# Performance work log

Hardware: AMD Instinct MI355X
Metric: run time of the kernel (lower is better)

## Reference

```python
import jax, jax.numpy as jnp
import numpy as np

DIM = 1024
NUM_HEADS = 16
HEAD_DIM = DIM // NUM_HEADS


def setup_inputs() -> dict:
    key = jax.random.key(0)
    k1, k2, k3 = jax.random.split(key, 3)
    x = jax.random.normal(k1, (2, 2048, DIM), dtype=jnp.float32)
    # nn.Linear weights stored as [out, in]; apply as x @ W.T
    w_qkv = jax.random.normal(k2, (3 * DIM, DIM), dtype=jnp.float32) * (1.0 / np.sqrt(DIM))
    w_out = jax.random.normal(k3, (DIM, DIM), dtype=jnp.float32) * (1.0 / np.sqrt(DIM))
    return {"x": x, "w_qkv": w_qkv, "w_out": w_out}


def reference(x, w_qkv, w_out):
    b, t, _ = x.shape
    qkv = x @ w_qkv.T                                  # [b, t, 3*dim]
    qkv = qkv.reshape(b, t, 3, NUM_HEADS, HEAD_DIM)    # (three h d) split order
    q, k, v = jnp.moveaxis(qkv, 2, 0)                  # each [b, t, h, d]
    q = q.transpose(0, 2, 1, 3)                        # [b, h, t, d]
    k = k.transpose(0, 2, 1, 3)
    v = v.transpose(0, 2, 1, 3)
    attn = jnp.einsum('bhid,bhjd->bhij', q, k) / np.sqrt(HEAD_DIM)
    causal_mask = jnp.triu(jnp.ones((t, t), dtype=bool), k=1)
    attn = jnp.where(causal_mask, -jnp.inf, attn)
    attn = jax.nn.softmax(attn, axis=-1)
    out = jnp.einsum('bhij,bhjd->bhid', attn, v)
    out = out.transpose(0, 2, 1, 3).reshape(b, t, DIM)
    return out @ w_out.T
```

## Files before the change

### kernel.cpp

```cpp
#include <hip/hip_runtime.h>

#define DIM_ 1024
#define HEADS_ 16
#define HD_ 64
#define T_ 2048
#define BATCH_ 2
#define QKVN_ 3072

typedef unsigned short u16;
typedef unsigned int u32;
typedef float f32x4 __attribute__((ext_vector_type(4)));
typedef float f32x16 __attribute__((ext_vector_type(16)));
typedef short s16x8 __attribute__((ext_vector_type(8)));
typedef unsigned short u16x4 __attribute__((ext_vector_type(4)));

__device__ __forceinline__ u16 f2bf(float f) {
  unsigned u = __float_as_uint(f);
  u += 0x7fffu + ((u >> 16) & 1u);
  return (u16)(u >> 16);
}

__device__ __forceinline__ float fexp2(float x) {
  float r;
  asm("v_exp_f32 %0, %1" : "=v"(r) : "v"(x));
  return r;
}

__device__ __forceinline__ u32 cvtpk(float a, float b) {
  u32 r;
  asm("v_cvt_pk_bf16_f32 %0, %1, %2" : "=v"(r) : "v"(a), "v"(b));
  return r;
}

__global__ __launch_bounds__(256) void cvt_all(const float* __restrict__ x,
                                               const float* __restrict__ wqkv,
                                               const float* __restrict__ wout,
                                               u16* __restrict__ outbase) {
  int i = blockIdx.x * 256 + threadIdx.x;
  const float4* src;
  int off;
  if (i < 1048576) { src = (const float4*)x; off = i; }
  else if (i < 1835008) { src = (const float4*)wqkv; off = i - 1048576; }
  else { src = (const float4*)wout; off = i - 1835008; }
  float4 v = src[off];
  u16x4 o;
  o.x = f2bf(v.x); o.y = f2bf(v.y); o.z = f2bf(v.z); o.w = f2bf(v.w);
  reinterpret_cast<u16x4*>(outbase)[i] = o;
}

__device__ __forceinline__ void gld_lds16(const void* g, void* l) {
  auto gp = (__attribute__((address_space(1))) char*)(unsigned long long)g;
  auto lp = (__attribute__((address_space(3))) char*)(unsigned int)(unsigned long long)l;
  __builtin_amdgcn_global_load_lds(gp, lp, 16, 0, 0);
}

template <int MODE>
__global__ __launch_bounds__(256) void gemm2(const u16* __restrict__ A,
                                             const u16* __restrict__ B,
                                             void* __restrict__ Cv,
                                             u16* __restrict__ vto,
                                             int N) {
  __shared__ __align__(16) u16 smem[17408];
  u16* As = smem;
  u16* Bs = smem + 8192;
  const int K = 1024;

  const int bid = blockIdx.x;
  const int cpx = gridDim.x >> 3;
  const int swz = (bid & 7) * cpx + (bid >> 3);
  const int nt = swz >> 5, mt = swz & 31;

  const int tid = threadIdx.x;
  const int lane = tid & 63;
  const int w = tid >> 6;
  const int wr = w >> 1, wc = w & 1;
  const int lrow = lane & 15, kg = lane >> 4;
  const u16* Ag = A + (size_t)(mt * 128) * K;
  const u16* Bg = B + (size_t)(nt * 128) * K;

  f32x4 acc[4][4];
#pragma unroll
  for (int i = 0; i < 4; ++i)
#pragma unroll
    for (int j = 0; j < 4; ++j) {
      f32x4 z = {0.f, 0.f, 0.f, 0.f};
      acc[i][j] = z;
    }

  const int e0 = tid * 8;
  const int row0 = e0 >> 5, kc0 = e0 & 31;
  const int row1 = row0 + 64, kc1 = kc0;
  const int ldsoff0 = (tid & ~63) * 16;
  const int ldsoff1 = (256 + (tid & ~63)) * 16;

  gld_lds16(Ag + (size_t)row0 * K + kc0, (char*)As + ldsoff0);
  gld_lds16(Ag + (size_t)row1 * K + kc1, (char*)As + ldsoff1);
  gld_lds16(Bg + (size_t)row0 * K + kc0, (char*)Bs + ldsoff0);
  gld_lds16(Bg + (size_t)row1 * K + kc1, (char*)Bs + ldsoff1);
  __syncthreads();

  int cur = 0;
  for (int k0 = 0; k0 < K; k0 += 32) {
    if (k0 + 32 < K) {
      const int nb = (cur ^ 1) * 8192;
      gld_lds16(Ag + (size_t)row0 * K + k0 + 32 + kc0, (char*)As + nb + ldsoff0);
      gld_lds16(Ag + (size_t)row1 * K + k0 + 32 + kc1, (char*)As + nb + ldsoff1);
      gld_lds16(Bg + (size_t)row0 * K + k0 + 32 + kc0, (char*)Bs + nb + ldsoff0);
      gld_lds16(Bg + (size_t)row1 * K + k0 + 32 + kc1, (char*)Bs + nb + ldsoff1);
    }
    const int cb = cur * 4096;
    s16x8 a[4], b[4];
#pragma unroll
    for (int mf = 0; mf < 4; ++mf)
      a[mf] = *(const s16x8*)&As[cb + (wr * 64 + mf * 16 + lrow) * 32 + 8 * kg];
#pragma unroll
    for (int nf = 0; nf < 4; ++nf)
      b[nf] = *(const s16x8*)&Bs[cb + (wc * 64 + nf * 16 + lrow) * 32 + 8 * kg];
#pragma unroll
    for (int mf = 0; mf < 4; ++mf)
#pragma unroll
      for (int nf = 0; nf < 4; ++nf)
        acc[mf][nf] = __builtin_amdgcn_mfma_f32_16x16x32_bf16(a[mf], b[nf], acc[mf][nf], 0, 0, 0);
    __syncthreads();
    cur ^= 1;
  }

  if (MODE == 1) {
    float* C = (float*)Cv;
#pragma unroll
    for (int mf = 0; mf < 4; ++mf)
#pragma unroll
      for (int nf = 0; nf < 4; ++nf)
#pragma unroll
        for (int j = 0; j < 4; ++j) {
          int r = mt * 128 + wr * 64 + mf * 16 + 4 * kg + j;
          int c = nt * 128 + wc * 64 + nf * 16 + lrow;
          C[(size_t)r * N + c] = acc[mf][nf][j];
        }
  } else if (nt < 16) {
    u16* qkvo = (u16*)Cv;
#pragma unroll
    for (int mf = 0; mf < 4; ++mf)
#pragma unroll
      for (int nf = 0; nf < 4; ++nf)
#pragma unroll
        for (int j = 0; j < 4; ++j) {
          int r = mt * 128 + wr * 64 + mf * 16 + 4 * kg + j;
          int c = nt * 128 + wc * 64 + nf * 16 + lrow;
          qkvo[(size_t)r * QKVN_ + c] = f2bf(acc[mf][nf][j]);
        }
  } else {
    u16* Vlds = smem;
#pragma unroll
    for (int mf = 0; mf < 4; ++mf)
#pragma unroll
      for (int nf = 0; nf < 4; ++nf) {
        const int cl = wc * 64 + nf * 16 + lrow;
        const int rl = wr * 64 + mf * 16 + 4 * kg;
#pragma unroll
        for (int j = 0; j < 4; ++j)
          Vlds[cl * 136 + rl + j] = f2bf(acc[mf][nf][j]);
      }
    __syncthreads();
    const int c16 = tid >> 4, chunk = tid & 15;
    const int bb = mt >> 4;
    const int tb = (mt & 15) * 128 + chunk * 8;
#pragma unroll
    for (int pass = 0; pass < 8; ++pass) {
      const int cl = pass * 16 + c16;
      const int cg = nt * 128 + cl;
      const int hV = (cg >> 6) & 15, d = cg & 63;
      const s16x8 v = *(const s16x8*)&Vlds[cl * 136 + chunk * 8];
      *(s16x8*)(vto + ((size_t)((bb * 16 + hV) * 64 + d)) * T_ + tb) = v;
    }
  }
}

__global__ __launch_bounds__(256, 2) void attn_fwd(const u16* __restrict__ qkv,
                                                   const u16* __restrict__ vt,
                                                   u16* __restrict__ o) {
  const int gid = blockIdx.x;
  const int pr = gid >> 5;
  const int bh = gid & 31;
  const int b = bh >> 4, h = bh & 15;
  const int tid = threadIdx.x;
  const int lane = tid & 63;
  const int qw = (tid >> 6) & 1;
  const int kvg = tid >> 7;
  const int l31 = lane & 31, hi = lane >> 5;

  __shared__ __align__(16) char smem[65536];

  const int row_s = tid >> 3, slot_s = tid & 7;
  const u16* Kbase = qkv + (size_t)(b * T_) * QKVN_ + 1024 + h * 64;
  const u16* Vbase = vt + (size_t)(bh * 64) * T_;
  const u16* KgA = Kbase + (size_t)row_s * QKVN_ + slot_s * 8;
  const u16* KgB = KgA + (size_t)32 * QKVN_;
  const u16* VgA = Vbase + (size_t)row_s * T_ + slot_s * 8;
  const u16* VgB = VgA + (size_t)32 * T_;
  const int dstA = row_s * 128 + ((slot_s ^ (row_s & 7)) << 4);

  const int rbyte = l31 * 128;
  const int xsw = l31 & 7;
  const float CEXP = 0.18033688011112042f;

  for (int ph = 0; ph < 2; ++ph) {
    const int jt = (ph == 0) ? (31 - pr) : pr;
    const int nt = jt + 1;
    const int nrt = (nt + 1) >> 1;
    const int qrow0 = 64 * jt + 32 * qw;

    s16x8 qf[4];
    {
      const u16* qp = qkv + (size_t)(b * T_ + qrow0 + l31) * QKVN_ + h * 64 + 8 * hi;
#pragma unroll
      for (int ksl = 0; ksl < 4; ++ksl)
        qf[ksl] = *(const s16x8*)(qp + 16 * ksl);
    }

    f32x16 o0v, o1v;
#pragma unroll
    for (int r = 0; r < 16; ++r) { o0v[r] = 0.f; o1v[r] = 0.f; }
    float mrun = -__builtin_inff(), lrun = 0.0f;

    __syncthreads();
    *(s16x8*)(smem + dstA)                 = *(const s16x8*)KgA;
    *(s16x8*)(smem + 4096 + dstA)          = *(const s16x8*)KgB;
    *(s16x8*)(smem + 32768 + dstA)         = *(const s16x8*)VgA;
    *(s16x8*)(smem + 32768 + 4096 + dstA)  = *(const s16x8*)VgB;
    if (nt > 1) {
      *(s16x8*)(smem + 8192 + dstA)                = *(const s16x8*)(KgA + (size_t)64 * QKVN_);
      *(s16x8*)(smem + 8192 + 4096 + dstA)         = *(const s16x8*)(KgB + (size_t)64 * QKVN_);
      *(s16x8*)(smem + 32768 + 8192 + dstA)        = *(const s16x8*)(VgA + 64);
      *(s16x8*)(smem + 32768 + 8192 + 4096 + dstA) = *(const s16x8*)(VgB + 64);
    }

    int cur = 0;
    for (int r = 0; r < nrt; ++r) {
      const int t = 2 * r + kvg;
      const bool pe = (2 * r + 2 < nt), po = (2 * r + 3 < nt);
      s16x8 ke0, ke1, ve0, ve1, ko0, ko1, vo0, vo1;
      if (pe) {
        const size_t kofs = (size_t)(2 * r + 2) * 64 * QKVN_;
        const int vofs = (2 * r + 2) * 64;
        ke0 = *(const s16x8*)(KgA + kofs);
        ke1 = *(const s16x8*)(KgB + kofs);
        ve0 = *(const s16x8*)(VgA + vofs);
        ve1 = *(const s16x8*)(VgB + vofs);
      }
      if (po) {
        const size_t kofs = (size_t)(2 * r + 3) * 64 * QKVN_;
        const int vofs = (2 * r + 3) * 64;
        ko0 = *(const s16x8*)(KgA + kofs);
        ko1 = *(const s16x8*)(KgB + kofs);
        vo0 = *(const s16x8*)(VgA + vofs);
        vo1 = *(const s16x8*)(VgB + vofs);
      }
      __syncthreads();

      if (t < nt) {
        const char* Kc = smem + cur * 16384 + kvg * 8192;
        const char* Vc = smem + 32768 + cur * 16384 + kvg * 8192;
        const bool isdiag = (t == nt - 1);
        const bool two = !(isdiag && qw == 0);

        f32x16 s0v, s1v;
#pragma unroll
        for (int rr = 0; rr < 16; ++rr) { s0v[rr] = 0.f; s1v[rr] = 0.f; }
        __builtin_amdgcn_s_setprio(1);
#pragma unroll
        for (int ksl = 0; ksl < 4; ++ksl) {
          const s16x8 kf = *(const s16x8*)(Kc + rbyte + (((2 * ksl + hi) ^ xsw) << 4));
          s0v = __builtin_amdgcn_mfma_f32_32x32x16_bf16(kf, qf[ksl], s0v, 0, 0, 0);
        }
        if (two) {
#pragma unroll
          for (int ksl = 0; ksl < 4; ++ksl) {
            const s16x8 kf = *(const s16x8*)(Kc + 4096 + rbyte + (((2 * ksl + hi) ^ xsw) << 4));
            s1v = __builtin_amdgcn_mfma_f32_32x32x16_bf16(kf, qf[ksl], s1v, 0, 0, 0);
          }
        }
        __builtin_amdgcn_s_setprio(0);

        if (isdiag) {
          const int thr = 32 * qw + l31;
#pragma unroll
          for (int rr = 0; rr < 16; ++rr) {
            const int kvl = 4 * hi + (rr & 3) + 8 * (rr >> 2);
            if (kvl > thr) s0v[rr] = -__builtin_inff();
            if (two && kvl + 32 > thr) s1v[rr] = -__builtin_inff();
          }
        }

        float mloc = s0v[0];
#pragma unroll
        for (int rr = 1; rr < 16; ++rr) mloc = fmaxf(mloc, s0v[rr]);
        if (two) {
#pragma unroll
          for (int rr = 0; rr < 16; ++rr) mloc = fmaxf(mloc, s1v[rr]);
        }
        mloc = fmaxf(mloc, __shfl_xor(mloc, 32));

        const bool needfull = !((mloc - mrun) * CEXP <= 8.0f);
        if (__any(needfull)) {
          const float newm = fmaxf(mrun, mloc);
          const float sc = fexp2((mrun - newm) * CEXP);
          mrun = newm;
          lrun *= sc;
          o0v *= sc;
          o1v *= sc;
        }
        const float msc = mrun * CEXP;

        float rs = 0.0f;
        u32 pd0[8], pd1[8];
#pragma unroll
        for (int ri = 0; ri < 8; ++ri) {
          const float p0 = fexp2(__builtin_fmaf(s0v[2 * ri], CEXP, -msc));
          const float p1 = fexp2(__builtin_fmaf(s0v[2 * ri + 1], CEXP, -msc));
          rs += p0 + p1;
          pd0[ri] = cvtpk(p0, p1);
        }
        if (two) {
#pragma unroll
          for (int ri = 0; ri < 8; ++ri) {
            const float p0 = fexp2(__builtin_fmaf(s1v[2 * ri], CEXP, -msc));
            const float p1 = fexp2(__builtin_fmaf(s1v[2 * ri + 1], CEXP, -msc));
            rs += p0 + p1;
            pd1[ri] = cvtpk(p0, p1);
          }
        }
        rs += __shfl_xor(rs, 32);
        lrun += rs;

        __builtin_amdgcn_s_setprio(1);
#pragma unroll
        for (int kk = 0; kk < 4; ++kk) {
          if (kk >= 2 && !two) break;
          u32 x0, y0, x1, y1;
          if (kk == 0)      { x0 = pd0[0]; y0 = pd0[2]; x1 = pd0[1]; y1 = pd0[3]; }
          else if (kk == 1) { x0 = pd0[4]; y0 = pd0[6]; x1 = pd0[5]; y1 = pd0[7]; }
          else if (kk == 2) { x0 = pd1[0]; y0 = pd1[2]; x1 = pd1[1]; y1 = pd1[3]; }
          else              { x0 = pd1[4]; y0 = pd1[6]; x1 = pd1[5]; y1 = pd1[7]; }
          asm volatile("v_permlane32_swap_b32 %0, %1" : "+v"(x0), "+v"(y0));
          asm volatile("v_permlane32_swap_b32 %0, %1" : "+v"(x1), "+v"(y1));
          u32 pw[4] = {x0, x1, y0, y1};
          const s16x8 pf = *(const s16x8*)pw;
          const s16x8 vf0 = *(const s16x8*)(Vc + rbyte + (((2 * kk + hi) ^ xsw) << 4));
          const s16x8 vf1 = *(const s16x8*)(Vc + 4096 + rbyte + (((2 * kk + hi) ^ xsw) << 4));
          o0v = __builtin_amdgcn_mfma_f32_32x32x16_bf16(vf0, pf, o0v, 0, 0, 0);
          o1v = __builtin_amdgcn_mfma_f32_32x32x16_bf16(vf1, pf, o1v, 0, 0, 0);
        }
        __builtin_amdgcn_s_setprio(0);
      }

      if (pe) {
        const int nb = (cur ^ 1) * 16384;
        *(s16x8*)(smem + nb + dstA)                = ke0;
        *(s16x8*)(smem + nb + 4096 + dstA)         = ke1;
        *(s16x8*)(smem + 32768 + nb + dstA)        = ve0;
        *(s16x8*)(smem + 32768 + nb + 4096 + dstA) = ve1;
      }
      if (po) {
        const int nb = (cur ^ 1) * 16384 + 8192;
        *(s16x8*)(smem + nb + dstA)                = ko0;
        *(s16x8*)(smem + nb + 4096 + dstA)         = ko1;
        *(s16x8*)(smem + 32768 + nb + dstA)        = vo0;
        *(s16x8*)(smem + 32768 + nb + 4096 + dstA) = vo1;
      }
      cur ^= 1;
    }

    __syncthreads();
    float* Om = (float*)smem + qw * 2048;
    float* Mf = (float*)(smem + 16384) + qw * 64;
    float* Lf = (float*)(smem + 16896) + qw * 64;
    if (kvg == 1) {
#pragma unroll
      for (int rr = 0; rr < 16; ++rr) {
        Om[rr * 64 + lane] = o0v[rr];
        Om[(16 + rr) * 64 + lane] = o1v[rr];
      }
      Mf[lane] = mrun;
      Lf[lane] = lrun;
    }
    __syncthreads();
    if (kvg == 0) {
      const float mA = Mf[lane];
      const float lA = Lf[lane];
      const float m2 = fmaxf(mrun, mA);
      const float sB = fexp2((mrun - m2) * CEXP);
      const float sA = fexp2((mA - m2) * CEXP);
      const float linv = 1.0f / (lrun * sB + lA * sA);
      u16* orow = o + (size_t)(b * T_ + qrow0 + l31) * DIM_ + h * 64;
#pragma unroll
      for (int ri = 0; ri < 8; ++ri) {
        const int dbase0 = 4 * hi + 8 * (ri >> 1) + 2 * (ri & 1);
        const float a0 = (o0v[2 * ri] * sB + Om[(2 * ri) * 64 + lane] * sA) * linv;
        const float a1 = (o0v[2 * ri + 1] * sB + Om[(2 * ri + 1) * 64 + lane] * sA) * linv;
        const float c0 = (o1v[2 * ri] * sB + Om[(16 + 2 * ri) * 64 + lane] * sA) * linv;
        const float c1 = (o1v[2 * ri + 1] * sB + Om[(16 + 2 * ri + 1) * 64 + lane] * sA) * linv;
        *(u32*)(orow + dbase0) = cvtpk(a0, a1);
        *(u32*)(orow + 32 + dbase0) = cvtpk(c0, c1);
      }
    }
  }
}

extern "C" void kernel_launch(void* const* d_in, const int* in_sizes, int n_in,
                              void* d_out, int out_size, void* d_ws, size_t ws_size,
                              hipStream_t stream) {
  const float* x = (const float*)d_in[0];
  const float* w_qkv = (const float*)d_in[1];
  const float* w_out = (const float*)d_in[2];
  char* ws = (char*)d_ws;
  u16* xb    = (u16*)(ws + 0);
  u16* wqkvb = (u16*)(ws + 8388608);
  u16* woutb = (u16*)(ws + 14680064);
  u16* qkvb  = (u16*)(ws + 16777216);
  u16* vtb   = (u16*)(ws + 41943040);
  u16* attno = (u16*)(ws + 50331648);

  cvt_all<<<8192, 256, 0, stream>>>(x, w_qkv, w_out, xb);
  gemm2<2><<<768, 256, 0, stream>>>(xb, wqkvb, qkvb, vtb, QKVN_);
  attn_fwd<<<512, 256, 0, stream>>>(qkvb, vtb, attno);
  gemm2<1><<<256, 256, 0, stream>>>(attno, woutb, d_out, nullptr, DIM_);
}
```

Measured before the change: 105.2 us.

## Single-buffer GEMM LDS and raise occupancy, split V transpose into halves

The GEMM kernel drops LDS double buffering so each tile is loaded and then synchronised before compute, roughly halving shared memory, and asks for 6 blocks per CU through launch bounds. The grid swizzle is replaced by a plain 2D grid, and the V-transpose epilogue now runs in two 64-column halves so it fits in the smaller LDS buffer, using packed 4-element stores. The intent is to hide memory latency through more resident waves instead of software prefetch. The cost is that load latency is no longer overlapped within a block, L2 locality from the swizzle is lost, and the register cap may cause spills.

```diff
diff --git a/kernel.cpp b/kernel.cpp
--- a/kernel.cpp
+++ b/kernel.cpp
@@ -55,21 +55,16 @@
 }
 
 template <int MODE>
-__global__ __launch_bounds__(256) void gemm2(const u16* __restrict__ A,
-                                             const u16* __restrict__ B,
-                                             void* __restrict__ Cv,
-                                             u16* __restrict__ vto,
-                                             int N) {
-  __shared__ __align__(16) u16 smem[17408];
+__global__ __launch_bounds__(256, 6) void gemm1(const u16* __restrict__ A,
+                                                const u16* __restrict__ B,
+                                                void* __restrict__ Cv,
+                                                u16* __restrict__ vto) {
+  constexpr int K = 1024;
+  constexpr int NN = (MODE == 1) ? 1024 : QKVN_;
+  __shared__ __align__(16) u16 smem[(MODE == 2) ? 8704 : 8192];
   u16* As = smem;
-  u16* Bs = smem + 8192;
-  const int K = 1024;
-
-  const int bid = blockIdx.x;
-  const int cpx = gridDim.x >> 3;
-  const int swz = (bid & 7) * cpx + (bid >> 3);
-  const int nt = swz >> 5, mt = swz & 31;
-
+  u16* Bs = smem + 4096;
+  const int nt = blockIdx.x, mt = blockIdx.y;
   const int tid = threadIdx.x;
   const int lane = tid & 63;
   const int w = tid >> 6;
@@ -93,36 +88,25 @@
   const int ldsoff0 = (tid & ~63) * 16;
   const int ldsoff1 = (256 + (tid & ~63)) * 16;
 
-  gld_lds16(Ag + (size_t)row0 * K + kc0, (char*)As + ldsoff0);
-  gld_lds16(Ag + (size_t)row1 * K + kc1, (char*)As + ldsoff1);
-  gld_lds16(Bg + (size_t)row0 * K + kc0, (char*)Bs + ldsoff0);
-  gld_lds16(Bg + (size_t)row1 * K + kc1, (char*)Bs + ldsoff1);
-  __syncthreads();
-
-  int cur = 0;
   for (int k0 = 0; k0 < K; k0 += 32) {
-    if (k0 + 32 < K) {
-      const int nb = (cur ^ 1) * 8192;
-      gld_lds16(Ag + (size_t)row0 * K + k0 + 32 + kc0, (char*)As + nb + ldsoff0);
-      gld_lds16(Ag + (size_t)row1 * K + k0 + 32 + kc1, (char*)As + nb + ldsoff1);
-      gld_lds16(Bg + (size_t)row0 * K + k0 + 32 + kc0, (char*)Bs + nb + ldsoff0);
-      gld_lds16(Bg + (size_t)row1 * K + k0 + 32 + kc1, (char*)Bs + nb + ldsoff1);
-    }
-    const int cb = cur * 4096;
+    gld_lds16(Ag + (size_t)row0 * K + k0 + kc0, (char*)As + ldsoff0);
+    gld_lds16(Ag + (size_t)row1 * K + k0 + kc1, (char*)As + ldsoff1);
+    gld_lds16(Bg + (size_t)row0 * K + k0 + kc0, (char*)Bs + ldsoff0);
+    gld_lds16(Bg + (size_t)row1 * K + k0 + kc1, (char*)Bs + ldsoff1);
+    __syncthreads();
     s16x8 a[4], b[4];
 #pragma unroll
     for (int mf = 0; mf < 4; ++mf)
-      a[mf] = *(const s16x8*)&As[cb + (wr * 64 + mf * 16 + lrow) * 32 + 8 * kg];
+      a[mf] = *(const s16x8*)&As[(wr * 64 + mf * 16 + lrow) * 32 + 8 * kg];
 #pragma unroll
     for (int nf = 0; nf < 4; ++nf)
-      b[nf] = *(const s16x8*)&Bs[cb + (wc * 64 + nf * 16 + lrow) * 32 + 8 * kg];
+      b[nf] = *(const s16x8*)&Bs[(wc * 64 + nf * 16 + lrow) * 32 + 8 * kg];
 #pragma unroll
     for (int mf = 0; mf < 4; ++mf)
 #pragma unroll
       for (int nf = 0; nf < 4; ++nf)
         acc[mf][nf] = __builtin_amdgcn_mfma_f32_16x16x32_bf16(a[mf], b[nf], acc[mf][nf], 0, 0, 0);
     __syncthreads();
-    cur ^= 1;
   }
 
   if (MODE == 1) {
@@ -135,7 +119,7 @@
         for (int j = 0; j < 4; ++j) {
           int r = mt * 128 + wr * 64 + mf * 16 + 4 * kg + j;
           int c = nt * 128 + wc * 64 + nf * 16 + lrow;
-          C[(size_t)r * N + c] = acc[mf][nf][j];
+          C[(size_t)r * NN + c] = acc[mf][nf][j];
         }
   } else if (nt < 16) {
     u16* qkvo = (u16*)Cv;
@@ -150,28 +134,34 @@
           qkvo[(size_t)r * QKVN_ + c] = f2bf(acc[mf][nf][j]);
         }
   } else {
-    u16* Vlds = smem;
-#pragma unroll
-    for (int mf = 0; mf < 4; ++mf)
-#pragma unroll
-      for (int nf = 0; nf < 4; ++nf) {
-        const int cl = wc * 64 + nf * 16 + lrow;
-        const int rl = wr * 64 + mf * 16 + 4 * kg;
-#pragma unroll
-        for (int j = 0; j < 4; ++j)
-          Vlds[cl * 136 + rl + j] = f2bf(acc[mf][nf][j]);
-      }
-    __syncthreads();
     const int c16 = tid >> 4, chunk = tid & 15;
     const int bb = mt >> 4;
     const int tb = (mt & 15) * 128 + chunk * 8;
 #pragma unroll
-    for (int pass = 0; pass < 8; ++pass) {
-      const int cl = pass * 16 + c16;
-      const int cg = nt * 128 + cl;
-      const int hV = (cg >> 6) & 15, d = cg & 63;
-      const s16x8 v = *(const s16x8*)&Vlds[cl * 136 + chunk * 8];
-      *(s16x8*)(vto + ((size_t)((bb * 16 + hV) * 64 + d)) * T_ + tb) = v;
+    for (int p = 0; p < 2; ++p) {
+      __syncthreads();
+      if (wc == p) {
+#pragma unroll
+        for (int mf = 0; mf < 4; ++mf)
+#pragma unroll
+          for (int nf = 0; nf < 4; ++nf) {
+            const int cl = nf * 16 + lrow;
+            const int rl = wr * 64 + mf * 16 + 4 * kg;
+            u16x4 pk;
+            pk.x = f2bf(acc[mf][nf][0]); pk.y = f2bf(acc[mf][nf][1]);
+            pk.z = f2bf(acc[mf][nf][2]); pk.w = f2bf(acc[mf][nf][3]);
+            *(u16x4*)&smem[cl * 136 + rl] = pk;
+          }
+      }
+      __syncthreads();
+#pragma unroll
+      for (int pp = 0; pp < 4; ++pp) {
+        const int cl = pp * 16 + c16;
+        const int cg = nt * 128 + p * 64 + cl;
+        const int hV = (cg >> 6) & 15, d = cg & 63;
+        const s16x8 v = *(const s16x8*)&smem[cl * 136 + chunk * 8];
+        *(s16x8*)(vto + ((size_t)((bb * 16 + hV) * 64 + d)) * T_ + tb) = v;
+      }
     }
   }
 }
@@ -422,7 +412,7 @@
   u16* attno = (u16*)(ws + 50331648);
 
   cvt_all<<<8192, 256, 0, stream>>>(x, w_qkv, w_out, xb);
-  gemm2<2><<<768, 256, 0, stream>>>(xb, wqkvb, qkvb, vtb, QKVN_);
+  gemm1<2><<<dim3(24, 32), 256, 0, stream>>>(xb, wqkvb, qkvb, vtb);
   attn_fwd<<<512, 256, 0, stream>>>(qkvb, vtb, attno);
-  gemm2<1><<<256, 256, 0, stream>>>(attno, woutb, d_out, nullptr, DIM_);
-}
+  gemm1<1><<<dim3(8, 32), 256, 0, stream>>>(attno, woutb, d_out, nullptr);
+}
```

New measurement: 227.4 us. +116.2%, slower.
